# Kernel tuning notes

Measured on AMD Instinct MI355X. Metric: run time of the kernel, lower is better.

## Reference

```python
import jax, jax.numpy as jnp
import numpy as np

N = 100000   # occupied voxels
C = 128      # input_dim
G = 64       # voxel grid extent per axis


def _build_neighbor_map(rng):
    # random unique voxel coords in a G^3 grid + hash lookup for 3x3x3 offsets
    lin = rng.choice(G ** 3, size=N, replace=False)
    coords = np.stack(np.unravel_index(lin, (G, G, G)), axis=1).astype(np.int64)  # [N,3]
    lut = np.full(G ** 3, -1, np.int32)
    lut[lin] = np.arange(N, dtype=np.int32)
    o = np.arange(-1, 2)
    offs = np.stack(np.meshgrid(o, o, o, indexing='ij'), -1).reshape(27, 3)  # [27,3]
    nc = coords[None, :, :] + offs[:, None, :]                 # [27,N,3]
    valid = ((nc >= 0) & (nc < G)).all(-1)                     # [27,N]
    nlin = (nc[..., 0] * G + nc[..., 1]) * G + nc[..., 2]
    nbr = np.where(valid, lut[np.clip(nlin, 0, G ** 3 - 1)], -1).astype(np.int32)
    return nbr


def setup_inputs() -> dict:
    rng = np.random.default_rng(0)
    nbr = _build_neighbor_map(rng)
    key = jax.random.key(0)
    ks = jax.random.split(key, 5)
    h = C // 2
    x = jax.random.normal(ks[0], (N, C), jnp.float32)
    w1 = jax.random.normal(ks[1], (C, C), jnp.float32) * 0.05
    b1 = jnp.zeros((C,), jnp.float32)
    w2 = jax.random.normal(ks[2], (C, C), jnp.float32) * 0.05
    b2 = jnp.zeros((C,), jnp.float32)
    rw1 = jax.random.normal(ks[3], (27, h, h), jnp.float32) * 0.05
    rb1 = jnp.zeros((h,), jnp.float32)
    rw2 = jax.random.normal(ks[4], (27, h, h), jnp.float32) * 0.05
    rb2 = jnp.zeros((h,), jnp.float32)
    return dict(x=x, w1=w1, b1=b1, w2=w2, b2=b2,
                rw1=rw1, rb1=rb1, rw2=rw2, rb2=rb2,
                nbr=jnp.asarray(nbr))


def _sconv3(feat, nbr, W, b):
    # sparse 3x3x3 conv: gather neighbor features per kernel offset, GEMM, sum
    mask = (nbr >= 0).astype(feat.dtype)                  # [27,N]
    g = feat[jnp.maximum(nbr, 0)] * mask[:, :, None]      # [27,N,c]
    return jnp.einsum('knc,kcd->nd', g, W) + b            # [N,c]


def reference(x, w1, b1, w2, b2, rw1, rb1, rw2, rb2, nbr):
    h = x.shape[1] // 2
    y = x @ w1 + b1                                       # conv1 (1x1x1)
    conv_x, trans_x = y[:, :h], y[:, h:]                  # split
    # resblock (stride 1 -> no skip conv): relu(conv)->relu(conv) + identity
    r = jax.nn.relu(_sconv3(conv_x, nbr, rw1, rb1))
    r = jax.nn.relu(_sconv3(r, nbr, rw2, rb2))
    conv_x = (r + conv_x) + conv_x                        # resblock(x) + x
    # CodedVTRBlock source unavailable: modeled as identity on trans branch
    res = jnp.concatenate([conv_x, trans_x], axis=1) @ w2 + b2  # conv2 (1x1x1)
    return x + res
```

## Files before the change

### kernel.cpp

```cpp
#include <hip/hip_runtime.h>


#define N_PTS 100000
#define NBLK128 782

typedef __attribute__((ext_vector_type(8))) short frag_ab;
typedef __attribute__((ext_vector_type(4))) float f32x4;
#define ZFRAG frag_ab{0, 0, 0, 0, 0, 0, 0, 0}

__device__ __forceinline__ unsigned short f2bf(float f) {
  union { float f; unsigned int i; } v; v.f = f;
  unsigned int r = v.i + 0x7fffu + ((v.i >> 16) & 1u);
  return (unsigned short)(r >> 16);
}
__device__ __forceinline__ float bf2f(unsigned short u) {
  union { unsigned int i; float f; } v; v.i = ((unsigned int)u) << 16; return v.f;
}

__device__ __forceinline__ void gload_lds16(const unsigned short* g, unsigned short* l) {
  __builtin_amdgcn_global_load_lds(
      (const __attribute__((address_space(1))) unsigned int*)g,
      (__attribute__((address_space(3))) unsigned int*)(unsigned int)(size_t)l,
      16, 0, 0);
}

__global__ __launch_bounds__(256) void k_prep(
    const float* __restrict__ w1, const float* __restrict__ w2,
    const float* __restrict__ rw1, const float* __restrict__ rw2,
    unsigned short* __restrict__ w1T, unsigned short* __restrict__ w2T,
    unsigned short* __restrict__ rw1T, unsigned short* __restrict__ rw2T) {
  int t = blockIdx.x * 256 + threadIdx.x;
  if (t < 128 * 128) {
    int c = t >> 7, d = t & 127;
    int pos = d * 128 + ((((c >> 3) ^ (d & 15)) << 3) | (c & 7));
    w1T[pos] = f2bf(w1[t]);
    w2T[pos] = f2bf(w2[t]);
  }
  if (t < 27 * 64 * 64) {
    int k = t >> 12, r = t & 4095, c = r >> 6, d = r & 63;
    int pos = (k << 12) + d * 64 + ((((c >> 3) ^ (d & 7)) << 3) | (c & 7));
    rw1T[pos] = f2bf(rw1[t]);
    rw2T[pos] = f2bf(rw2[t]);
  }
}

__global__ __launch_bounds__(256) void k_gemm_in(
    const float* __restrict__ x, const unsigned short* __restrict__ w1T,
    const float* __restrict__ b1, unsigned short* __restrict__ y) {
  __shared__ unsigned short sw[16384];
  const int tid = threadIdx.x, lane = tid & 63, w = tid >> 6;
  const int m16 = lane & 15, q = lane >> 4;
#pragma unroll
  for (int r = 0; r < 8; ++r) {
    const int off = (w * 8 + r) * 512 + lane * 8;
    gload_lds16(w1T + off, &sw[off]);
  }
  __syncthreads();
  const int rowbase = blockIdx.x * 128 + w * 32;
  f32x4 acc[2][8] = {};
#pragma unroll
  for (int kk = 0; kk < 4; ++kk) {
    frag_ab a[2];
#pragma unroll
    for (int rt = 0; rt < 2; ++rt) {
      int r0 = rowbase + rt * 16 + m16;
      int rc = r0 < N_PTS ? r0 : N_PTS - 1;
      const float* xp = x + (size_t)rc * 128 + kk * 32 + q * 8;
      float4 f0 = *(const float4*)xp;
      float4 f1 = *(const float4*)(xp + 4);
      frag_ab t;
      t[0] = (short)f2bf(f0.x); t[1] = (short)f2bf(f0.y);
      t[2] = (short)f2bf(f0.z); t[3] = (short)f2bf(f0.w);
      t[4] = (short)f2bf(f1.x); t[5] = (short)f2bf(f1.y);
      t[6] = (short)f2bf(f1.z); t[7] = (short)f2bf(f1.w);
      a[rt] = t;
    }
#pragma unroll
    for (int ct = 0; ct < 8; ++ct) {
      const int d = ct * 16 + m16;
      const int phys = ((kk << 2) | q) ^ m16;
      frag_ab bf = *(const frag_ab*)(&sw[d * 128 + phys * 8]);
      acc[0][ct] = __builtin_amdgcn_mfma_f32_16x16x32_bf16(a[0], bf, acc[0][ct], 0, 0, 0);
      acc[1][ct] = __builtin_amdgcn_mfma_f32_16x16x32_bf16(a[1], bf, acc[1][ct], 0, 0, 0);
    }
  }
#pragma unroll
  for (int ct = 0; ct < 8; ++ct) {
    const int col = ct * 16 + m16;
    const float bias = b1[col];
#pragma unroll
    for (int rt = 0; rt < 2; ++rt)
#pragma unroll
      for (int j = 0; j < 4; ++j) {
        int r = rowbase + rt * 16 + q * 4 + j;
        if (r < N_PTS) y[(size_t)r * 128 + col] = f2bf(acc[rt][ct][j] + bias);
      }
  }
}

template <bool FUSE>
__global__ __launch_bounds__(256) void k_conv(
    const unsigned short* __restrict__ feat, const int fstride,
    const int* __restrict__ nbr,
    const unsigned short* __restrict__ rwT, const float* __restrict__ rb,
    const unsigned short* __restrict__ res, unsigned short* __restrict__ out) {
  __shared__ unsigned short sw[2][4096];
  const int tid = threadIdx.x, lane = tid & 63, w = tid >> 6;
  const int m16 = lane & 15, q = lane >> 4;
  const int rowbase = blockIdx.x * 128 + w * 32;
  const int p0 = rowbase + m16, p1 = p0 + 16;
  const bool v0 = p0 < N_PTS, v1 = p1 < N_PTS;
  const int s0 = w * 1024 + lane * 8;
  const int s1 = s0 + 512;

  int i0r[2], i1r[2];
  i0r[0] = v0 ? nbr[p0] : -1;
  i1r[0] = v1 ? nbr[p1] : -1;
  i0r[1] = v0 ? nbr[N_PTS + p0] : -1;
  i1r[1] = v1 ? nbr[N_PTS + p1] : -1;

  frag_ab A[2][2][2];
#pragma unroll
  for (int a = 0; a < 2; ++a)
#pragma unroll
    for (int b = 0; b < 2; ++b)
#pragma unroll
      for (int c = 0; c < 2; ++c) A[a][b][c] = ZFRAG;

  {
    const unsigned short* src = rwT;
    gload_lds16(src + s0, &sw[0][s0]);
    gload_lds16(src + s1, &sw[0][s1]);
    if (i0r[0] >= 0) {
      const unsigned short* fp = feat + (size_t)i0r[0] * fstride + q * 8;
      A[0][0][0] = *(const frag_ab*)fp; A[0][0][1] = *(const frag_ab*)(fp + 32);
    }
    if (i1r[0] >= 0) {
      const unsigned short* fp = feat + (size_t)i1r[0] * fstride + q * 8;
      A[0][1][0] = *(const frag_ab*)fp; A[0][1][1] = *(const frag_ab*)(fp + 32);
    }
  }
  __syncthreads();

  f32x4 acc[2][4] = {};
#pragma unroll
  for (int k = 0; k < 27; ++k) {
    const int b = k & 1;
    if (k + 1 < 27) {
      const unsigned short* src = rwT + ((k + 1) << 12);
      gload_lds16(src + s0, &sw[b ^ 1][s0]);
      gload_lds16(src + s1, &sw[b ^ 1][s1]);
      const int n = (k + 1) & 1;
      int j0 = i0r[n], j1 = i1r[n];
      A[n][0][0] = ZFRAG; A[n][0][1] = ZFRAG; A[n][1][0] = ZFRAG; A[n][1][1] = ZFRAG;
      if (j0 >= 0) {
        const unsigned short* fp = feat + (size_t)j0 * fstride + q * 8;
        A[n][0][0] = *(const frag_ab*)fp; A[n][0][1] = *(const frag_ab*)(fp + 32);
      }
      if (j1 >= 0) {
        const unsigned short* fp = feat + (size_t)j1 * fstride + q * 8;
        A[n][1][0] = *(const frag_ab*)fp; A[n][1][1] = *(const frag_ab*)(fp + 32);
      }
    }
    if (k + 2 < 27) {
      i0r[k & 1] = v0 ? nbr[(k + 2) * N_PTS + p0] : -1;
      i1r[k & 1] = v1 ? nbr[(k + 2) * N_PTS + p1] : -1;
    }
#pragma unroll
    for (int kk = 0; kk < 2; ++kk)
#pragma unroll
      for (int ct = 0; ct < 4; ++ct) {
        const int d = ct * 16 + m16;
        const int phys = ((kk << 2) | q) ^ (m16 & 7);
        frag_ab bf = *(const frag_ab*)(&sw[b][d * 64 + phys * 8]);
        acc[0][ct] = __builtin_amdgcn_mfma_f32_16x16x32_bf16(A[b][0][kk], bf, acc[0][ct], 0, 0, 0);
        acc[1][ct] = __builtin_amdgcn_mfma_f32_16x16x32_bf16(A[b][1][kk], bf, acc[1][ct], 0, 0, 0);
      }
    __syncthreads();
  }

#pragma unroll
  for (int ct = 0; ct < 4; ++ct) {
    const int col = ct * 16 + m16;
    const float bias = rb[col];
#pragma unroll
    for (int rt = 0; rt < 2; ++rt)
#pragma unroll
      for (int j = 0; j < 4; ++j) {
        const int r = rowbase + rt * 16 + q * 4 + j;
        if (r < N_PTS) {
          float v = acc[rt][ct][j] + bias;
          v = v > 0.f ? v : 0.f;
          if constexpr (FUSE) v += 2.f * bf2f(res[(size_t)r * 128 + col]);
          out[(size_t)r * 64 + col] = f2bf(v);
        }
      }
  }
}

__global__ __launch_bounds__(256) void k_gemm_out(
    const float* __restrict__ x, const unsigned short* __restrict__ z1,
    const unsigned short* __restrict__ y, const unsigned short* __restrict__ w2T,
    const float* __restrict__ b2, float* __restrict__ out) {
  __shared__ unsigned short sw[16384];
  const int tid = threadIdx.x, lane = tid & 63, w = tid >> 6;
  const int m16 = lane & 15, q = lane >> 4;
#pragma unroll
  for (int r = 0; r < 8; ++r) {
    const int off = (w * 8 + r) * 512 + lane * 8;
    gload_lds16(w2T + off, &sw[off]);
  }
  __syncthreads();
  const int rowbase = blockIdx.x * 128 + w * 32;
  f32x4 acc[2][8] = {};
#pragma unroll
  for (int kk = 0; kk < 4; ++kk) {
    frag_ab a[2];
#pragma unroll
    for (int rt = 0; rt < 2; ++rt) {
      int r0 = rowbase + rt * 16 + m16;
      int rc = r0 < N_PTS ? r0 : N_PTS - 1;
      const unsigned short* ap = (kk < 2)
          ? (z1 + (size_t)rc * 64 + kk * 32 + q * 8)
          : (y + (size_t)rc * 128 + 64 + (kk - 2) * 32 + q * 8);
      a[rt] = *(const frag_ab*)ap;
    }
#pragma unroll
    for (int ct = 0; ct < 8; ++ct) {
      const int d = ct * 16 + m16;
      const int phys = ((kk << 2) | q) ^ m16;
      frag_ab bf = *(const frag_ab*)(&sw[d * 128 + phys * 8]);
      acc[0][ct] = __builtin_amdgcn_mfma_f32_16x16x32_bf16(a[0], bf, acc[0][ct], 0, 0, 0);
      acc[1][ct] = __builtin_amdgcn_mfma_f32_16x16x32_bf16(a[1], bf, acc[1][ct], 0, 0, 0);
    }
  }
#pragma unroll
  for (int ct = 0; ct < 8; ++ct) {
    const int col = ct * 16 + m16;
    const float bias = b2[col];
#pragma unroll
    for (int rt = 0; rt < 2; ++rt)
#pragma unroll
      for (int j = 0; j < 4; ++j) {
        int r = rowbase + rt * 16 + q * 4 + j;
        if (r < N_PTS) {
          size_t o = (size_t)r * 128 + col;
          out[o] = acc[rt][ct][j] + bias + x[o];
        }
      }
  }
}

extern "C" void kernel_launch(void* const* d_in, const int* in_sizes, int n_in,
                              void* d_out, int out_size, void* d_ws, size_t ws_size,
                              hipStream_t stream) {
  const float* x   = (const float*)d_in[0];
  const float* w1  = (const float*)d_in[1];
  const float* b1  = (const float*)d_in[2];
  const float* w2  = (const float*)d_in[3];
  const float* b2  = (const float*)d_in[4];
  const float* rw1 = (const float*)d_in[5];
  const float* rb1 = (const float*)d_in[6];
  const float* rw2 = (const float*)d_in[7];
  const float* rb2 = (const float*)d_in[8];
  const int* nbr = (const int*)d_in[9];
  float* out = (float*)d_out;

  char* ws = (char*)d_ws;
  unsigned short* w1T  = (unsigned short*)(ws);
  unsigned short* w2T  = (unsigned short*)(ws + 32768);
  unsigned short* rw1T = (unsigned short*)(ws + 65536);
  unsigned short* rw2T = (unsigned short*)(ws + 286720);
  unsigned short* y    = (unsigned short*)(ws + 507904);
  unsigned short* r1   = (unsigned short*)(ws + 507904 + 25600000);
  unsigned short* z1   = (unsigned short*)(ws + 507904 + 38400000);

  k_prep<<<432, 256, 0, stream>>>(w1, w2, rw1, rw2, w1T, w2T, rw1T, rw2T);
  k_gemm_in<<<NBLK128, 256, 0, stream>>>(x, w1T, b1, y);
  k_conv<false><<<NBLK128, 256, 0, stream>>>(y, 128, nbr, rw1T, rb1, nullptr, r1);
  k_conv<true><<<NBLK128, 256, 0, stream>>>(r1, 64, nbr, rw2T, rb2, y, z1);
  k_gemm_out<<<NBLK128, 256, 0, stream>>>(x, z1, y, w2T, b2, out);
}
```

Before: 243.1 us.

## Process two kernel offsets per pipeline stage in sparse conv

Restructures the 27-offset loop in the sparse 3x3x3 conv kernel so each pipeline stage stages weights and gathers neighbor features for two offsets at once. It double-buffers pairs of weight tiles in LDS. This halves the number of __syncthreads barriers and puts more gather loads in flight per stage to hide gather latency. In exchange it doubles LDS use per block and raises register pressure from the larger A fragment and index arrays, which may reduce occupancy.

```diff
diff --git a/kernel.cpp b/kernel.cpp
--- a/kernel.cpp
+++ b/kernel.cpp
@@ -104,7 +104,7 @@
     const int* __restrict__ nbr,
     const unsigned short* __restrict__ rwT, const float* __restrict__ rb,
     const unsigned short* __restrict__ res, unsigned short* __restrict__ out) {
-  __shared__ unsigned short sw[2][4096];
+  __shared__ unsigned short sw[2][2][4096];
   const int tid = threadIdx.x, lane = tid & 63, w = tid >> 6;
   const int m16 = lane & 15, q = lane >> 4;
   const int rowbase = blockIdx.x * 128 + w * 32;
@@ -113,71 +113,89 @@
   const int s0 = w * 1024 + lane * 8;
   const int s1 = s0 + 512;
 
-  int i0r[2], i1r[2];
-  i0r[0] = v0 ? nbr[p0] : -1;
-  i1r[0] = v1 ? nbr[p1] : -1;
-  i0r[1] = v0 ? nbr[N_PTS + p0] : -1;
-  i1r[1] = v1 ? nbr[N_PTS + p1] : -1;
-
-  frag_ab A[2][2][2];
-#pragma unroll
-  for (int a = 0; a < 2; ++a)
-#pragma unroll
-    for (int b = 0; b < 2; ++b)
-#pragma unroll
-      for (int c = 0; c < 2; ++c) A[a][b][c] = ZFRAG;
-
-  {
-    const unsigned short* src = rwT;
-    gload_lds16(src + s0, &sw[0][s0]);
-    gload_lds16(src + s1, &sw[0][s1]);
-    if (i0r[0] >= 0) {
-      const unsigned short* fp = feat + (size_t)i0r[0] * fstride + q * 8;
-      A[0][0][0] = *(const frag_ab*)fp; A[0][0][1] = *(const frag_ab*)(fp + 32);
-    }
-    if (i1r[0] >= 0) {
-      const unsigned short* fp = feat + (size_t)i1r[0] * fstride + q * 8;
-      A[0][1][0] = *(const frag_ab*)fp; A[0][1][1] = *(const frag_ab*)(fp + 32);
-    }
-  }
+  int I[2][2][2];
+  frag_ab A[2][2][2][2];
+  f32x4 acc[2][4] = {};
+
+#define STAGE(buf, o, koff)                                                     \
+  {                                                                             \
+    const unsigned short* src = rwT + ((size_t)(koff) << 12);                   \
+    unsigned short* dst = &sw[buf][o][0];                                       \
+    gload_lds16(src + s0, dst + s0);                                            \
+    gload_lds16(src + s1, dst + s1);                                            \
+  }
+
+#define IDXLOAD(pp, o, koff)                                                    \
+  {                                                                             \
+    I[pp][o][0] = v0 ? nbr[(size_t)(koff) * N_PTS + p0] : -1;                   \
+    I[pp][o][1] = v1 ? nbr[(size_t)(koff) * N_PTS + p1] : -1;                   \
+  }
+
+#define GATHER(pp, o)                                                           \
+  {                                                                             \
+    A[pp][o][0][0] = ZFRAG; A[pp][o][0][1] = ZFRAG;                             \
+    A[pp][o][1][0] = ZFRAG; A[pp][o][1][1] = ZFRAG;                             \
+    const int j0 = I[pp][o][0], j1 = I[pp][o][1];                               \
+    if (j0 >= 0) {                                                              \
+      const unsigned short* fp = feat + (size_t)j0 * fstride + q * 8;           \
+      A[pp][o][0][0] = *(const frag_ab*)fp;                                     \
+      A[pp][o][0][1] = *(const frag_ab*)(fp + 32);                              \
+    }                                                                           \
+    if (j1 >= 0) {                                                              \
+      const unsigned short* fp = feat + (size_t)j1 * fstride + q * 8;           \
+      A[pp][o][1][0] = *(const frag_ab*)fp;                                     \
+      A[pp][o][1][1] = *(const frag_ab*)(fp + 32);                              \
+    }                                                                           \
+  }
+
+#define COMPUTE(cur, o)                                                         \
+  _Pragma("unroll") for (int kk = 0; kk < 2; ++kk)                              \
+    _Pragma("unroll") for (int ct = 0; ct < 4; ++ct) {                          \
+      const int d = ct * 16 + m16;                                              \
+      const int phys = ((kk << 2) | q) ^ (m16 & 7);                             \
+      frag_ab bf = *(const frag_ab*)(&sw[cur][o][d * 64 + phys * 8]);           \
+      acc[0][ct] = __builtin_amdgcn_mfma_f32_16x16x32_bf16(A[cur][o][0][kk], bf, acc[0][ct], 0, 0, 0); \
+      acc[1][ct] = __builtin_amdgcn_mfma_f32_16x16x32_bf16(A[cur][o][1][kk], bf, acc[1][ct], 0, 0, 0); \
+    }
+
+  IDXLOAD(0, 0, 0); IDXLOAD(0, 1, 1);
+  IDXLOAD(1, 0, 2); IDXLOAD(1, 1, 3);
+  STAGE(0, 0, 0); STAGE(0, 1, 1);
+  GATHER(0, 0); GATHER(0, 1);
   __syncthreads();
 
-  f32x4 acc[2][4] = {};
-#pragma unroll
-  for (int k = 0; k < 27; ++k) {
-    const int b = k & 1;
-    if (k + 1 < 27) {
-      const unsigned short* src = rwT + ((k + 1) << 12);
-      gload_lds16(src + s0, &sw[b ^ 1][s0]);
-      gload_lds16(src + s1, &sw[b ^ 1][s1]);
-      const int n = (k + 1) & 1;
-      int j0 = i0r[n], j1 = i1r[n];
-      A[n][0][0] = ZFRAG; A[n][0][1] = ZFRAG; A[n][1][0] = ZFRAG; A[n][1][1] = ZFRAG;
-      if (j0 >= 0) {
-        const unsigned short* fp = feat + (size_t)j0 * fstride + q * 8;
-        A[n][0][0] = *(const frag_ab*)fp; A[n][0][1] = *(const frag_ab*)(fp + 32);
+  for (int pout = 0; pout < 6; ++pout) {
+#pragma unroll
+    for (int u = 0; u < 2; ++u) {
+      const int p = pout * 2 + u;
+      const int nxt = u ^ 1;
+      STAGE(nxt, 0, 2 * p + 2);
+      STAGE(nxt, 1, 2 * p + 3);
+      if (p < 11) {
+        IDXLOAD(u, 0, 2 * p + 4);
+        IDXLOAD(u, 1, 2 * p + 5);
+      } else {
+        IDXLOAD(u, 0, 26);
       }
-      if (j1 >= 0) {
-        const unsigned short* fp = feat + (size_t)j1 * fstride + q * 8;
-        A[n][1][0] = *(const frag_ab*)fp; A[n][1][1] = *(const frag_ab*)(fp + 32);
-      }
-    }
-    if (k + 2 < 27) {
-      i0r[k & 1] = v0 ? nbr[(k + 2) * N_PTS + p0] : -1;
-      i1r[k & 1] = v1 ? nbr[(k + 2) * N_PTS + p1] : -1;
-    }
-#pragma unroll
-    for (int kk = 0; kk < 2; ++kk)
-#pragma unroll
-      for (int ct = 0; ct < 4; ++ct) {
-        const int d = ct * 16 + m16;
-        const int phys = ((kk << 2) | q) ^ (m16 & 7);
-        frag_ab bf = *(const frag_ab*)(&sw[b][d * 64 + phys * 8]);
-        acc[0][ct] = __builtin_amdgcn_mfma_f32_16x16x32_bf16(A[b][0][kk], bf, acc[0][ct], 0, 0, 0);
-        acc[1][ct] = __builtin_amdgcn_mfma_f32_16x16x32_bf16(A[b][1][kk], bf, acc[1][ct], 0, 0, 0);
-      }
-    __syncthreads();
-  }
+      GATHER(nxt, 0);
+      GATHER(nxt, 1);
+      COMPUTE(u, 0);
+      COMPUTE(u, 1);
+      __syncthreads();
+    }
+  }
+
+  STAGE(1, 0, 26);
+  GATHER(1, 0);
+  COMPUTE(0, 0);
+  COMPUTE(0, 1);
+  __syncthreads();
+  COMPUTE(1, 0);
+
+#undef STAGE
+#undef IDXLOAD
+#undef GATHER
+#undef COMPUTE
 
 #pragma unroll
   for (int ct = 0; ct < 4; ++ct) {
```

After: 258.0 us. 1.06x slower.
